# Performance work log

Hardware: AMD Instinct MI355X
Metric: run time of the kernel (lower is better)

The kernel has to match this reference:

```python
import jax, jax.numpy as jnp
import numpy as np

HEADS = 8
HC = 64  # num_head_channels
DIM = 256
HIDDEN = HEADS * HC
EPS = 1e-5


def setup_inputs() -> dict:
    key = jax.random.key(0)
    ks = jax.random.split(key, 6)
    x = jax.random.normal(ks[0], (16, DIM, 64, 64), dtype=jnp.float32)
    Wq = jax.random.normal(ks[1], (HIDDEN, DIM), dtype=jnp.float32) * 0.02
    Wk = jax.random.normal(ks[2], (HIDDEN, DIM), dtype=jnp.float32) * 0.02
    Wv = jax.random.normal(ks[3], (HIDDEN, DIM), dtype=jnp.float32) * 0.02
    Wo = jax.random.normal(ks[4], (DIM, HIDDEN), dtype=jnp.float32) * 0.02
    bo = jnp.zeros((DIM,), dtype=jnp.float32)
    gamma = jnp.ones((DIM,), dtype=jnp.float32)
    beta = jnp.zeros((DIM,), dtype=jnp.float32)
    return {"x": x, "Wq": Wq, "Wk": Wk, "Wv": Wv, "Wo": Wo, "bo": bo,
            "gamma": gamma, "beta": beta}


def reference(x, Wq, Wk, Wv, Wo, bo, gamma, beta):
    b, c, h, w = x.shape
    n = h * w
    scale = HC ** (-0.5)
    xf = x.reshape(b, c, n)  # [b, c, n]
    # 1x1 convs == channel matmuls
    q = jnp.einsum('oc,bcn->bon', Wq, xf).reshape(b * HEADS, HC, n)
    k = jnp.einsum('oc,bcn->bon', Wk, xf).reshape(b * HEADS, HC, n)
    v = jnp.einsum('oc,bcn->bon', Wv, xf).reshape(b * HEADS, HC, n)
    q = jax.nn.softmax(q, axis=1) * scale      # softmax over head channels
    k = jax.nn.softmax(k, axis=2)              # softmax over spatial
    # context = k @ v^T : [bh, hc, hc]
    context = jnp.einsum('bdn,ben->bde', k, v)
    # output = context^T @ q : [bh, hc, n]
    out = jnp.einsum('bde,bdn->ben', context, q)
    out = out.reshape(b, HIDDEN, n)
    # to_out conv1x1 + bias
    y = jnp.einsum('oc,bcn->bon', Wo, out) + bo[None, :, None]
    # GroupNorm(num_groups=1): normalize over (c, n) per sample
    mean = jnp.mean(y, axis=(1, 2), keepdims=True)
    var = jnp.var(y, axis=(1, 2), keepdims=True)
    y = (y - mean) * jax.lax.rsqrt(var + EPS)
    y = y * gamma[None, :, None] + beta[None, :, None]
    return y.reshape(b, c, h, w) + x
```

## Files before the change

### kernel.cpp

```cpp
#include <hip/hip_runtime.h>
#include <hip/hip_bf16.h>

#define DEV __device__ __forceinline__

constexpr int B_ = 16, CDIM = 256, NDIM = 4096, HID = 512, HEADS = 8, HC = 64;
constexpr float EPSV = 1e-5f;

using bf16x8 = __attribute__((ext_vector_type(8))) __bf16;
using f32x4  = __attribute__((ext_vector_type(4))) float;
using s16x8  = __attribute__((ext_vector_type(8))) short;
using s16x4  = __attribute__((ext_vector_type(4))) short;

DEV short f2bf(float f) {
  __hip_bfloat16 h = __float2bfloat16(f);
  return *reinterpret_cast<short*>(&h);
}
DEV float bf2f(short s) {
  union { unsigned u; float f; } c;
  c.u = ((unsigned)(unsigned short)s) << 16;
  return c.f;
}
DEV f32x4 MFMA(bf16x8 a, bf16x8 b, f32x4 c) {
  return __builtin_amdgcn_mfma_f32_16x16x32_bf16(a, b, c, 0, 0, 0);
}

__global__ void wconv_kernel(const float* __restrict__ Wq, const float* __restrict__ Wk,
                             const float* __restrict__ Wv, const float* __restrict__ Wo,
                             short* __restrict__ Wall, short* __restrict__ Wo_b) {
  const int i = blockIdx.x * 256 + threadIdx.x;
  const int nw = HID * CDIM;
  if (i < nw) Wall[i] = f2bf(Wq[i]);
  else if (i < 2 * nw) Wall[i] = f2bf(Wk[i - nw]);
  else if (i < 3 * nw) Wall[i] = f2bf(Wv[i - 2 * nw]);
  if (i < CDIM * HID) Wo_b[i] = f2bf(Wo[i]);
}

__global__ __launch_bounds__(256) void xconv_kernel(const float* __restrict__ x, short* __restrict__ xt) {
  __shared__ float t[32][33];
  const int bi = blockIdx.z, n0 = blockIdx.x * 32, c0 = blockIdx.y * 32;
  const int tx = threadIdx.x, ty = threadIdx.y;
  const float* xb = x + (size_t)bi * CDIM * NDIM;
#pragma unroll
  for (int i = 0; i < 32; i += 8)
    t[ty + i][tx] = xb[(size_t)(c0 + ty + i) * NDIM + n0 + tx];
  __syncthreads();
  short* xtb = xt + (size_t)bi * NDIM * CDIM;
#pragma unroll
  for (int i = 0; i < 32; i += 8)
    xtb[(size_t)(n0 + ty + i) * CDIM + c0 + tx] = f2bf(t[tx][ty + i]);
}

DEV bf16x8 xs_read(const char* xs, int row, int colShorts) {
  int byte = (row << 9) + (colShorts << 1);
  byte ^= (row & 7) << 4;
  return *(const bf16x8*)(xs + byte);
}
DEV bf16x8 t128_read(const char* t, int row, int colShorts) {
  int byte = (row << 7) + (colShorts << 1);
  byte ^= (row & 7) << 4;
  return *(const bf16x8*)(t + byte);
}

__global__ __launch_bounds__(256) void kvslice_kernel(const short* __restrict__ Wall,
                                                      const short* __restrict__ xt,
                                                      float* __restrict__ ctxp,
                                                      float* __restrict__ statp,
                                                      int nper) {
  const int bh = blockIdx.x, sl = blockIdx.y, nsl = gridDim.y;
  const int bi = bh >> 3, h = bh & 7;
  const int tid = threadIdx.x, lane = tid & 63, wid = tid >> 6;
  const int ro = lane & 15, g = lane >> 4, ko = g * 8;
  const short* Wk = Wall + (size_t)(HID + h * HC) * CDIM;
  const short* Wv = Wall + (size_t)(2 * HID + h * HC) * CDIM;
  const char* xbase = (const char*)(xt + ((size_t)bi * NDIM + (size_t)sl * nper) * CDIM);
  __shared__ __align__(16) char xs[64 * 512];
  __shared__ short pl[64][68];
  __shared__ short vl[64][68];
  bf16x8 ak[8], av[8];
#pragma unroll
  for (int ks = 0; ks < 8; ++ks) {
    ak[ks] = *(const bf16x8*)&Wk[(size_t)(wid * 16 + ro) * CDIM + ks * 32 + ko];
    av[ks] = *(const bf16x8*)&Wv[(size_t)(wid * 16 + ro) * CDIM + ks * 32 + ko];
  }
  float sacc[4] = {0.f, 0.f, 0.f, 0.f};
  f32x4 cacc[4] = {};
  const int drow = wid * 16 + g * 4;
  s16x8 r[8];
#pragma unroll
  for (int it = 0; it < 8; ++it) r[it] = *(const s16x8*)(xbase + it * 4096 + tid * 16);
  for (int nc = 0; nc < nper; nc += 64) {
    if (nc > 0) {
#pragma unroll
      for (int ks = 0; ks < 2; ++ks) {
        bf16x8 pa = *(const bf16x8*)&pl[wid * 16 + ro][ks * 32 + ko];
#pragma unroll
        for (int et = 0; et < 4; ++et) {
          bf16x8 vb = *(const bf16x8*)&vl[et * 16 + ro][ks * 32 + ko];
          cacc[et] = MFMA(pa, vb, cacc[et]);
        }
      }
    }
#pragma unroll
    for (int it = 0; it < 8; ++it) {
      const int fb = it * 4096 + tid * 16;
      *(s16x8*)(xs + (fb ^ (((fb >> 9) & 7) << 4))) = r[it];
    }
    __syncthreads();
    if (nc + 64 < nper) {
      const char* srcn = xbase + (size_t)(nc + 64) * 512;
#pragma unroll
      for (int it = 0; it < 8; ++it) r[it] = *(const s16x8*)(srcn + it * 4096 + tid * 16);
    }
    f32x4 kacc[4] = {};
    f32x4 vacc[4] = {};
#pragma unroll
    for (int ks = 0; ks < 8; ++ks)
#pragma unroll
      for (int nt = 0; nt < 4; ++nt) {
        bf16x8 bfr = xs_read(xs, nt * 16 + ro, ks * 32 + ko);
        kacc[nt] = MFMA(ak[ks], bfr, kacc[nt]);
        vacc[nt] = MFMA(av[ks], bfr, vacc[nt]);
      }
#pragma unroll
    for (int nt = 0; nt < 4; ++nt)
#pragma unroll
      for (int j = 0; j < 4; ++j) {
        const float p = __expf(kacc[nt][j]);
        sacc[j] += p;
        pl[drow + j][nt * 16 + ro] = f2bf(p);
        vl[drow + j][nt * 16 + ro] = f2bf(vacc[nt][j]);
      }
    __syncthreads();
  }
#pragma unroll
  for (int ks = 0; ks < 2; ++ks) {
    bf16x8 pa = *(const bf16x8*)&pl[wid * 16 + ro][ks * 32 + ko];
#pragma unroll
    for (int et = 0; et < 4; ++et) {
      bf16x8 vb = *(const bf16x8*)&vl[et * 16 + ro][ks * 32 + ko];
      cacc[et] = MFMA(pa, vb, cacc[et]);
    }
  }
#pragma unroll
  for (int o = 1; o < 16; o <<= 1)
#pragma unroll
    for (int j = 0; j < 4; ++j) sacc[j] += __shfl_xor(sacc[j], o);
  float* cp = ctxp + ((size_t)bh * nsl + sl) * HC * HC;
#pragma unroll
  for (int et = 0; et < 4; ++et)
#pragma unroll
    for (int j = 0; j < 4; ++j)
      cp[(drow + j) * HC + et * 16 + ro] = cacc[et][j];
  if (ro == 0) {
    float* sp = statp + ((size_t)bh * nsl + sl) * HC;
#pragma unroll
    for (int j = 0; j < 4; ++j) sp[drow + j] = sacc[j];
  }
}

__global__ __launch_bounds__(256) void qsm_kernel(const short* __restrict__ Wall,
                                                  const short* __restrict__ xt,
                                                  short* __restrict__ qtc,
                                                  int NC, int nbase) {
  const int bi = blockIdx.y, n0 = blockIdx.x * 64;
  const int tid = threadIdx.x, lane = tid & 63, wid = tid >> 6;
  const int ro = lane & 15, g = lane >> 4, ko = g * 8;
  __shared__ __align__(16) char xs[64 * 512];
  __shared__ float ps[8 * 4 * 4 * 16];
  const char* xbase = (const char*)(xt + ((size_t)bi * NDIM + nbase + n0) * CDIM);
#pragma unroll
  for (int it = 0; it < 8; ++it) {
    const int fb = it * 4096 + tid * 16;
    *(s16x8*)(xs + (fb ^ (((fb >> 9) & 7) << 4))) = *(const s16x8*)(xbase + fb);
  }
  __syncthreads();
  const short* wbase = Wall + (size_t)(wid * 16 + ro) * CDIM + ko;
  bf16x8 aq[8], aqn[8];
#pragma unroll
  for (int ks = 0; ks < 8; ++ks) aq[ks] = *(const bf16x8*)(wbase + ks * 32);
#pragma unroll 1
  for (int h = 0; h < HEADS; ++h) {
    if (h < 7) {
      const short* wn = wbase + (size_t)(h + 1) * HC * CDIM;
#pragma unroll
      for (int ks = 0; ks < 8; ++ks) aqn[ks] = *(const bf16x8*)(wn + ks * 32);
    }
    f32x4 kacc[4] = {};
#pragma unroll
    for (int ks = 0; ks < 8; ++ks)
#pragma unroll
      for (int nt = 0; nt < 4; ++nt)
        kacc[nt] = MFMA(aq[ks], xs_read(xs, nt * 16 + ro, ks * 32 + ko), kacc[nt]);
    float tsum[4];
#pragma unroll
    for (int nt = 0; nt < 4; ++nt) {
#pragma unroll
      for (int j = 0; j < 4; ++j) kacc[nt][j] = __expf(kacc[nt][j]);
      tsum[nt] = kacc[nt][0] + kacc[nt][1] + kacc[nt][2] + kacc[nt][3];
    }
#pragma unroll
    for (int nt = 0; nt < 4; ++nt) {
      tsum[nt] += __shfl_xor(tsum[nt], 16);
      tsum[nt] += __shfl_xor(tsum[nt], 32);
    }
    if (g == 0) {
#pragma unroll
      for (int nt = 0; nt < 4; ++nt) ps[((h * 4 + wid) * 4 + nt) * 16 + ro] = tsum[nt];
    }
    __syncthreads();
    float inv[4];
#pragma unroll
    for (int nt = 0; nt < 4; ++nt) {
      const float t = ps[((h * 4 + 0) * 4 + nt) * 16 + ro] + ps[((h * 4 + 1) * 4 + nt) * 16 + ro] +
                      ps[((h * 4 + 2) * 4 + nt) * 16 + ro] + ps[((h * 4 + 3) * 4 + nt) * 16 + ro];
      inv[nt] = 0.125f / t;
    }
    short* qh = qtc + ((size_t)bi * NC + n0) * HID + h * HC + wid * 16 + g * 4;
#pragma unroll
    for (int nt = 0; nt < 4; ++nt) {
      s16x4 v;
#pragma unroll
      for (int j = 0; j < 4; ++j) v[j] = f2bf(kacc[nt][j] * inv[nt]);
      *(s16x4*)(qh + (size_t)(nt * 16 + ro) * HID) = v;
    }
#pragma unroll
    for (int ks = 0; ks < 8; ++ks) aq[ks] = aqn[ks];
  }
}

__global__ __launch_bounds__(256) void ctxred_kernel(const float* __restrict__ ctxp,
                                                     const float* __restrict__ statp,
                                                     short* __restrict__ ctx, int nsl) {
  const int bh = blockIdx.x, tid = threadIdx.x;
  const int d = tid >> 2, e0 = (tid & 3) * 16;
  const float* sp = statp + (size_t)bh * nsl * HC;
  float stot = 0.f;
  for (int i = 0; i < nsl; ++i) stot += sp[i * HC + d];
  const float inv = 1.f / stot;
  const float* cp = ctxp + (size_t)bh * nsl * HC * HC;
  short* cb = ctx + (size_t)bh * HC * HC;
  for (int e = e0; e < e0 + 16; ++e) {
    float u = 0.f;
    for (int i = 0; i < nsl; ++i) u += cp[i * HC * HC + d * HC + e];
    cb[d * HC + e] = f2bf(u * inv);
  }
}

__global__ __launch_bounds__(256) void meff_kernel(const short* __restrict__ Wo_b,
                                                   const short* __restrict__ ctx,
                                                   short* __restrict__ Meff) {
  const int bh = blockIdx.x, bi = bh >> 3, h = bh & 7;
  const int tid = threadIdx.x, lane = tid & 63, wid = tid >> 6;
  const int ro = lane & 15, ko = (lane >> 4) * 8;
  const short* Arow = Wo_b + h * HC;
  const short* Bc = ctx + (size_t)bh * HC * HC;
  f32x4 acc[4][4] = {};
#pragma unroll
  for (int ks = 0; ks < 64; ks += 32) {
    bf16x8 af[4], bv[4];
#pragma unroll
    for (int mi = 0; mi < 4; ++mi)
      af[mi] = *(const bf16x8*)&Arow[(size_t)(wid * 64 + mi * 16 + ro) * HID + ks + ko];
#pragma unroll
    for (int ni = 0; ni < 4; ++ni)
      bv[ni] = *(const bf16x8*)&Bc[(ni * 16 + ro) * HC + ks + ko];
#pragma unroll
    for (int mi = 0; mi < 4; ++mi)
#pragma unroll
      for (int ni = 0; ni < 4; ++ni) acc[mi][ni] = MFMA(af[mi], bv[ni], acc[mi][ni]);
  }
  short* Mb = Meff + (size_t)bi * CDIM * HID + h * HC;
  const int r0 = wid * 64 + ((lane >> 4) << 2), c0 = lane & 15;
#pragma unroll
  for (int mi = 0; mi < 4; ++mi)
#pragma unroll
    for (int ni = 0; ni < 4; ++ni)
#pragma unroll
      for (int j = 0; j < 4; ++j)
        Mb[(size_t)(r0 + mi * 16 + j) * HID + ni * 16 + c0] = f2bf(acc[mi][ni][j]);
}

template <bool BF16OUT>
__global__ __launch_bounds__(256) void ymm_kernel(const short* __restrict__ Meff,
                                                  const short* __restrict__ qtc,
                                                  const float* __restrict__ bo,
                                                  void* __restrict__ yout,
                                                  float2* __restrict__ partials,
                                                  int NC, int nbase, int pbase) {
  constexpr int K = HID;
  __shared__ __align__(16) char Al[128 * 128];
  __shared__ __align__(16) char Bl[128 * 128];
  __shared__ float a1[4], a2[4];
  const int bi = blockIdx.z, mt = blockIdx.y, nt = blockIdx.x;
  const int tid = threadIdx.x, lane = tid & 63, wid = tid >> 6;
  const int wr = (wid >> 1) * 64, wc = (wid & 1) * 64;
  const char* Ab = (const char*)(Meff + (size_t)bi * CDIM * HID + (size_t)mt * 128 * K);
  const char* Bb = (const char*)(qtc + ((size_t)bi * NC + (size_t)nt * 128) * K);
  f32x4 acc[4][4] = {};
  const int ro = lane & 15, ko = (lane >> 4) * 8;
  for (int kt = 0; kt < K; kt += 64) {
    const char* As = Ab + kt * 2;
    const char* Bs = Bb + kt * 2;
#pragma unroll
    for (int it = 0; it < 4; ++it) {
      const int fb = it * 4096 + tid * 16;
      const int row = fb >> 7, inner = fb & 127;
      const int swz = fb ^ ((row & 7) << 4);
      *(s16x8*)(Al + swz) = *(const s16x8*)(As + (size_t)row * 1024 + inner);
      *(s16x8*)(Bl + swz) = *(const s16x8*)(Bs + (size_t)row * 1024 + inner);
    }
    __syncthreads();
#pragma unroll
    for (int ks = 0; ks < 64; ks += 32) {
      bf16x8 af[4], bfr[4];
#pragma unroll
      for (int i = 0; i < 4; ++i) {
        af[i]  = t128_read(Al, wr + i * 16 + ro, ks + ko);
        bfr[i] = t128_read(Bl, wc + i * 16 + ro, ks + ko);
      }
#pragma unroll
      for (int mi = 0; mi < 4; ++mi)
#pragma unroll
        for (int ni = 0; ni < 4; ++ni)
          acc[mi][ni] = MFMA(af[mi], bfr[ni], acc[mi][ni]);
    }
    __syncthreads();
  }
  const int r0 = mt * 128 + wr + ((lane >> 4) << 2);
  const int c0 = nbase + nt * 128 + wc + ro;
  float s1 = 0.f, s2 = 0.f;
#pragma unroll
  for (int mi = 0; mi < 4; ++mi)
#pragma unroll
    for (int j = 0; j < 4; ++j) {
      const int row = r0 + mi * 16 + j;
      const float b = bo[row];
#pragma unroll
      for (int ni = 0; ni < 4; ++ni) {
        const float v = acc[mi][ni][j] + b;
        if constexpr (BF16OUT)
          ((short*)yout)[(size_t)bi * CDIM * NDIM + (size_t)row * NDIM + c0 + ni * 16] = f2bf(v);
        else
          ((float*)yout)[(size_t)bi * CDIM * NDIM + (size_t)row * NDIM + c0 + ni * 16] = v;
        s1 += v;
        s2 += v * v;
      }
    }
#pragma unroll
  for (int o = 1; o < 64; o <<= 1) { s1 += __shfl_xor(s1, o); s2 += __shfl_xor(s2, o); }
  if (lane == 0) { a1[wid] = s1; a2[wid] = s2; }
  __syncthreads();
  if (tid == 0)
    partials[bi * 64 + pbase + mt * gridDim.x + nt] =
        make_float2(a1[0] + a1[1] + a1[2] + a1[3], a2[0] + a2[1] + a2[2] + a2[3]);
}

__global__ void redstats_kernel(const float2* __restrict__ partials, float* __restrict__ stats) {
  const int bi = blockIdx.x, l = threadIdx.x;
  float2 p = partials[bi * 64 + l];
  float s1 = p.x, s2 = p.y;
#pragma unroll
  for (int o = 32; o; o >>= 1) { s1 += __shfl_xor(s1, o); s2 += __shfl_xor(s2, o); }
  if (l == 0) { stats[bi * 2] = s1; stats[bi * 2 + 1] = s2; }
}

template <bool YBF>
__global__ __launch_bounds__(256) void final_kernel(const void* __restrict__ ysrc, float* __restrict__ dst,
                                                    const float* __restrict__ x,
                                                    const float* __restrict__ gamma, const float* __restrict__ beta,
                                                    const float* __restrict__ stats) {
  const int bi = blockIdx.y;
  constexpr float invN = 1.f / ((float)CDIM * NDIM);
  const float mean = stats[bi * 2] * invN;
  const float var = stats[bi * 2 + 1] * invN - mean * mean;
  const float rstd = rsqrtf(var + EPSV);
  float4* d4 = (float4*)(dst + (size_t)bi * CDIM * NDIM);
  const float4* x4 = (const float4*)(x + (size_t)bi * CDIM * NDIM);
  for (int i = blockIdx.x * 256 + threadIdx.x; i < CDIM * NDIM / 4; i += 128 * 256) {
    const int c = i >> 10;
    const float g = gamma[c] * rstd;
    const float b = beta[c] - mean * g;
    float4 v;
    if constexpr (YBF) {
      s16x4 yv = *(const s16x4*)((const short*)ysrc + (size_t)bi * CDIM * NDIM + (size_t)i * 4);
      v.x = bf2f(yv[0]); v.y = bf2f(yv[1]); v.z = bf2f(yv[2]); v.w = bf2f(yv[3]);
    } else {
      v = ((const float4*)((const float*)ysrc + (size_t)bi * CDIM * NDIM))[i];
    }
    const float4 xv = x4[i];
    v.x = v.x * g + b + xv.x;
    v.y = v.y * g + b + xv.y;
    v.z = v.z * g + b + xv.z;
    v.w = v.w * g + b + xv.w;
    d4[i] = v;
  }
}

extern "C" void kernel_launch(void* const* d_in, const int* in_sizes, int n_in,
                              void* d_out, int out_size, void* d_ws, size_t ws_size,
                              hipStream_t stream) {
  const float* x     = (const float*)d_in[0];
  const float* Wq    = (const float*)d_in[1];
  const float* Wk    = (const float*)d_in[2];
  const float* Wv    = (const float*)d_in[3];
  const float* Wo    = (const float*)d_in[4];
  const float* bo    = (const float*)d_in[5];
  const float* gamma = (const float*)d_in[6];
  const float* beta  = (const float*)d_in[7];
  float* out = (float*)d_out;

  char* w = (char*)d_ws;
  size_t off = 0;
  auto alloc = [&](size_t n) {
    char* p = w + off;
    off = (off + n + 255) & ~(size_t)255;
    return p;
  };
  constexpr int NSL = 8;
  short* xt    = (short*)alloc((size_t)B_ * NDIM * CDIM * 2);
  short* Wall  = (short*)alloc((size_t)3 * HID * CDIM * 2);
  short* Wo_b  = (short*)alloc((size_t)CDIM * HID * 2);
  short* ctx   = (short*)alloc((size_t)128 * HC * HC * 2);
  short* Meff  = (short*)alloc((size_t)B_ * CDIM * HID * 2);
  float2* partials = (float2*)alloc((size_t)B_ * 64 * sizeof(float2));
  float* stats = (float*)alloc(32 * 4);
  float* ctxp  = (float*)alloc((size_t)128 * NSL * HC * HC * 4);
  float* statp = (float*)alloc((size_t)128 * NSL * HC * 4);
  const size_t base = off;

  int NC = 4096;
  while (NC > 64 && base + (size_t)B_ * NC * HID * 2 > ws_size) NC >>= 1;
  short* qtc = (short*)alloc((size_t)B_ * NC * HID * 2);
  const size_t ybf_bytes = (size_t)B_ * CDIM * NDIM * 2;
  const bool use_ybf = (off + ybf_bytes) <= ws_size;
  short* ybf = use_ybf ? (short*)alloc(ybf_bytes) : nullptr;

  wconv_kernel<<<1536, 256, 0, stream>>>(Wq, Wk, Wv, Wo, Wall, Wo_b);
  xconv_kernel<<<dim3(128, 8, B_), dim3(32, 8), 0, stream>>>(x, xt);
  kvslice_kernel<<<dim3(128, NSL), 256, 0, stream>>>(Wall, xt, ctxp, statp, NDIM / NSL);
  ctxred_kernel<<<128, 256, 0, stream>>>(ctxp, statp, ctx, NSL);
  meff_kernel<<<128, 256, 0, stream>>>(Wo_b, ctx, Meff);
  const int nchunks = NDIM / NC;
  for (int c = 0; c < nchunks; ++c) {
    qsm_kernel<<<dim3(NC / 64, B_), 256, 0, stream>>>(Wall, xt, qtc, NC, c * NC);
    if (use_ybf)
      ymm_kernel<true><<<dim3(NC / 128, 2, B_), 256, 0, stream>>>(Meff, qtc, bo, ybf, partials,
                                                                  NC, c * NC, c * 2 * (NC / 128));
    else
      ymm_kernel<false><<<dim3(NC / 128, 2, B_), 256, 0, stream>>>(Meff, qtc, bo, out, partials,
                                                                   NC, c * NC, c * 2 * (NC / 128));
  }
  redstats_kernel<<<B_, 64, 0, stream>>>(partials, stats);
  if (use_ybf)
    final_kernel<true><<<dim3(128, B_), 256, 0, stream>>>(ybf, out, x, gamma, beta, stats);
  else
    final_kernel<false><<<dim3(128, B_), 256, 0, stream>>>(out, out, x, gamma, beta, stats);
}
```

Before: 219.2 us.

## Fuse context reduction into Meff kernel and remap block indices for cache locality

Merges the context partial-sum reduction and the Wo·ctx product into one kernel that stages the normalized context in shared memory, removing a launch and the global round-trip of ctx. It also remaps kvslice block indices so blocks with the same head run together, and adds a swizzled block-to-tile mapping in ymm that spreads batches across the linear launch order, likely to even out load across XCDs and caches. The remapping is hardcoded to the full-size grid and is enabled only when NC is 4096.

```diff
diff --git a/kernel.cpp b/kernel.cpp
--- a/kernel.cpp
+++ b/kernel.cpp
@@ -66,8 +66,9 @@
                                                       float* __restrict__ ctxp,
                                                       float* __restrict__ statp,
                                                       int nper) {
-  const int bh = blockIdx.x, sl = blockIdx.y, nsl = gridDim.y;
-  const int bi = bh >> 3, h = bh & 7;
+  const int phys = blockIdx.x, sl = blockIdx.y, nsl = gridDim.y;
+  const int h = phys >> 4, bi = phys & 15;
+  const int bh = bi * 8 + h;
   const int tid = threadIdx.x, lane = tid & 63, wid = tid >> 6;
   const int ro = lane & 15, g = lane >> 4, ko = g * 8;
   const short* Wk = Wall + (size_t)(HID + h * HC) * CDIM;
@@ -228,32 +229,36 @@
   }
 }
 
-__global__ __launch_bounds__(256) void ctxred_kernel(const float* __restrict__ ctxp,
-                                                     const float* __restrict__ statp,
-                                                     short* __restrict__ ctx, int nsl) {
-  const int bh = blockIdx.x, tid = threadIdx.x;
-  const int d = tid >> 2, e0 = (tid & 3) * 16;
-  const float* sp = statp + (size_t)bh * nsl * HC;
-  float stot = 0.f;
-  for (int i = 0; i < nsl; ++i) stot += sp[i * HC + d];
-  const float inv = 1.f / stot;
-  const float* cp = ctxp + (size_t)bh * nsl * HC * HC;
-  short* cb = ctx + (size_t)bh * HC * HC;
-  for (int e = e0; e < e0 + 16; ++e) {
-    float u = 0.f;
-    for (int i = 0; i < nsl; ++i) u += cp[i * HC * HC + d * HC + e];
-    cb[d * HC + e] = f2bf(u * inv);
-  }
-}
-
-__global__ __launch_bounds__(256) void meff_kernel(const short* __restrict__ Wo_b,
-                                                   const short* __restrict__ ctx,
-                                                   short* __restrict__ Meff) {
+__global__ __launch_bounds__(256) void cmred_kernel(const float* __restrict__ ctxp,
+                                                    const float* __restrict__ statp,
+                                                    const short* __restrict__ Wo_b,
+                                                    short* __restrict__ Meff, int nsl) {
   const int bh = blockIdx.x, bi = bh >> 3, h = bh & 7;
   const int tid = threadIdx.x, lane = tid & 63, wid = tid >> 6;
   const int ro = lane & 15, ko = (lane >> 4) * 8;
+  __shared__ short cl[64][68];
+  {
+    const int d = tid >> 2, eb = (tid & 3) * 16;
+    const float* sp = statp + (size_t)bh * nsl * HC;
+    float stot = 0.f;
+    for (int i = 0; i < nsl; ++i) stot += sp[i * HC + d];
+    const float inv = 1.f / stot;
+    const float* cp = ctxp + (size_t)bh * nsl * HC * HC + d * HC + eb;
+#pragma unroll
+    for (int e4 = 0; e4 < 16; e4 += 4) {
+      float u0 = 0.f, u1 = 0.f, u2 = 0.f, u3 = 0.f;
+      for (int i = 0; i < nsl; ++i) {
+        const float4 c = *(const float4*)&cp[i * HC * HC + e4];
+        u0 += c.x; u1 += c.y; u2 += c.z; u3 += c.w;
+      }
+      cl[d][eb + e4 + 0] = f2bf(u0 * inv);
+      cl[d][eb + e4 + 1] = f2bf(u1 * inv);
+      cl[d][eb + e4 + 2] = f2bf(u2 * inv);
+      cl[d][eb + e4 + 3] = f2bf(u3 * inv);
+    }
+  }
+  __syncthreads();
   const short* Arow = Wo_b + h * HC;
-  const short* Bc = ctx + (size_t)bh * HC * HC;
   f32x4 acc[4][4] = {};
 #pragma unroll
   for (int ks = 0; ks < 64; ks += 32) {
@@ -263,7 +268,7 @@
       af[mi] = *(const bf16x8*)&Arow[(size_t)(wid * 64 + mi * 16 + ro) * HID + ks + ko];
 #pragma unroll
     for (int ni = 0; ni < 4; ++ni)
-      bv[ni] = *(const bf16x8*)&Bc[(ni * 16 + ro) * HC + ks + ko];
+      bv[ni] = *(const bf16x8*)&cl[ni * 16 + ro][ks + ko];
 #pragma unroll
     for (int mi = 0; mi < 4; ++mi)
 #pragma unroll
@@ -286,12 +291,21 @@
                                                   const float* __restrict__ bo,
                                                   void* __restrict__ yout,
                                                   float2* __restrict__ partials,
-                                                  int NC, int nbase, int pbase) {
+                                                  int NC, int nbase, int pbase, int swz) {
   constexpr int K = HID;
   __shared__ __align__(16) char Al[128 * 128];
   __shared__ __align__(16) char Bl[128 * 128];
   __shared__ float a1[4], a2[4];
-  const int bi = blockIdx.z, mt = blockIdx.y, nt = blockIdx.x;
+  int bi, mt, nt;
+  if (swz) {
+    const int lin = blockIdx.x + 32 * blockIdx.y + 64 * blockIdx.z;
+    bi = ((lin & 7) << 1) | (lin >> 9);
+    const int rest = (lin >> 3) & 63;
+    mt = rest >> 5;
+    nt = rest & 31;
+  } else {
+    bi = blockIdx.z; mt = blockIdx.y; nt = blockIdx.x;
+  }
   const int tid = threadIdx.x, lane = tid & 63, wid = tid >> 6;
   const int wr = (wid >> 1) * 64, wc = (wid & 1) * 64;
   const char* Ab = (const char*)(Meff + (size_t)bi * CDIM * HID + (size_t)mt * 128 * K);
@@ -305,9 +319,9 @@
     for (int it = 0; it < 4; ++it) {
       const int fb = it * 4096 + tid * 16;
       const int row = fb >> 7, inner = fb & 127;
-      const int swz = fb ^ ((row & 7) << 4);
-      *(s16x8*)(Al + swz) = *(const s16x8*)(As + (size_t)row * 1024 + inner);
-      *(s16x8*)(Bl + swz) = *(const s16x8*)(Bs + (size_t)row * 1024 + inner);
+      const int swb = fb ^ ((row & 7) << 4);
+      *(s16x8*)(Al + swb) = *(const s16x8*)(As + (size_t)row * 1024 + inner);
+      *(s16x8*)(Bl + swb) = *(const s16x8*)(Bs + (size_t)row * 1024 + inner);
     }
     __syncthreads();
 #pragma unroll
@@ -420,7 +434,6 @@
   short* xt    = (short*)alloc((size_t)B_ * NDIM * CDIM * 2);
   short* Wall  = (short*)alloc((size_t)3 * HID * CDIM * 2);
   short* Wo_b  = (short*)alloc((size_t)CDIM * HID * 2);
-  short* ctx   = (short*)alloc((size_t)128 * HC * HC * 2);
   short* Meff  = (short*)alloc((size_t)B_ * CDIM * HID * 2);
   float2* partials = (float2*)alloc((size_t)B_ * 64 * sizeof(float2));
   float* stats = (float*)alloc(32 * 4);
@@ -438,17 +451,17 @@
   wconv_kernel<<<1536, 256, 0, stream>>>(Wq, Wk, Wv, Wo, Wall, Wo_b);
   xconv_kernel<<<dim3(128, 8, B_), dim3(32, 8), 0, stream>>>(x, xt);
   kvslice_kernel<<<dim3(128, NSL), 256, 0, stream>>>(Wall, xt, ctxp, statp, NDIM / NSL);
-  ctxred_kernel<<<128, 256, 0, stream>>>(ctxp, statp, ctx, NSL);
-  meff_kernel<<<128, 256, 0, stream>>>(Wo_b, ctx, Meff);
+  cmred_kernel<<<128, 256, 0, stream>>>(ctxp, statp, Wo_b, Meff, NSL);
   const int nchunks = NDIM / NC;
   for (int c = 0; c < nchunks; ++c) {
+    const int swz = (NC == 4096) ? 1 : 0;
     qsm_kernel<<<dim3(NC / 64, B_), 256, 0, stream>>>(Wall, xt, qtc, NC, c * NC);
     if (use_ybf)
       ymm_kernel<true><<<dim3(NC / 128, 2, B_), 256, 0, stream>>>(Meff, qtc, bo, ybf, partials,
-                                                                  NC, c * NC, c * 2 * (NC / 128));
+                                                                  NC, c * NC, c * 2 * (NC / 128), swz);
     else
       ymm_kernel<false><<<dim3(NC / 128, 2, B_), 256, 0, stream>>>(Meff, qtc, bo, out, partials,
-                                                                   NC, c * NC, c * 2 * (NC / 128));
+                                                                   NC, c * NC, c * 2 * (NC / 128), swz);
   }
   redstats_kernel<<<B_, 64, 0, stream>>>(partials, stats);
   if (use_ybf)
```

Result: faster. 196.3 us (-10.5%).
